# Optimization experiments

Hardware: AMD Instinct MI355X
Metric: run time of the kernel (lower is better)

## Reference

```python
import jax, jax.numpy as jnp
import numpy as np

B, A, NBH, F, G, H = 8, 512, 64, 128, 50, 8
DH = F // H
CUTOFF = 5.0


def setup_inputs() -> dict:
    key = jax.random.key(0)
    ks = jax.random.split(key, 13)
    x = jax.random.normal(ks[0], (B, A, F), jnp.float32)
    e = jax.random.normal(ks[1], (B, A, F), jnp.float32)
    t = jax.random.normal(ks[2], (B, F), jnp.float32)
    # distances in [0, 1.2*cutoff] so some pairs fall outside the cutoff
    r_ij = jax.random.uniform(ks[3], (B, A, NBH), jnp.float32) * (1.2 * CUTOFF)
    f_ij = jax.random.normal(ks[4], (B, A, NBH, G), jnp.float32)
    neighbors = jax.random.randint(ks[5], (B, A, NBH), 0, A, jnp.int32)
    neighbor_mask = jax.random.randint(ks[6], (B, A, NBH), 0, 2, jnp.int32).astype(bool)
    sF = 1.0 / np.sqrt(F).astype(np.float32)
    W_filt = jax.random.normal(ks[7], (G, F), jnp.float32) * (1.0 / np.sqrt(G).astype(np.float32))
    b_filt = jnp.zeros((F,), jnp.float32)
    Wq = jax.random.normal(ks[8], (F, F), jnp.float32) * sF
    Wk = jax.random.normal(ks[9], (F, F), jnp.float32) * sF
    Wv = jax.random.normal(ks[10], (F, F), jnp.float32) * sF
    Wo = jax.random.normal(ks[11], (F, F), jnp.float32) * sF
    bo = jnp.zeros((F,), jnp.float32)
    return dict(e=e, x=x, t=t, r_ij=r_ij, f_ij=f_ij,
                W_filt=W_filt, b_filt=b_filt, Wq=Wq, Wk=Wk, Wv=Wv, Wo=Wo, bo=bo,
                neighbors=neighbors, neighbor_mask=neighbor_mask)


def reference(e, x, t, r_ij, f_ij, W_filt, b_filt, Wq, Wk, Wv, Wo, bo,
              neighbors, neighbor_mask):
    # ---- filter network + cosine cutoff: W (B, A, NBH, F) ----
    W = f_ij @ W_filt + b_filt
    C = 0.5 * (jnp.cos(jnp.pi * r_ij / CUTOFF) + 1.0)
    C = C * (r_ij < CUTOFF).astype(x.dtype)           # (B, A, NBH)
    W = W * C[..., None]

    # ---- neighbor gather: nbh (B, A, NBH, F) ----
    bidx = jnp.arange(B)[:, None, None]
    nbh = x[bidx, neighbors]                           # irregular gather
    nbh = nbh * W                                      # filter-modulated messages

    # ---- EgoAttention: central atom queries its neighbors ----
    q = (x @ Wq).reshape(B, A, H, DH)                  # bahd
    k = (nbh @ Wk).reshape(B, A, NBH, H, DH)           # banhd
    v = (nbh @ Wv).reshape(B, A, NBH, H, DH)
    scale = np.float32(1.0 / np.sqrt(DH))
    scores = jnp.einsum('bahd,banhd->bahn', q, k) * scale
    scores = jnp.where(neighbor_mask[:, :, None, :], scores, jnp.float32(-1e9))
    attn = jax.nn.softmax(scores, axis=-1)             # over neighbors
    msg = jnp.einsum('bahn,banhd->bahd', attn, v).reshape(B, A, F)
    v_out = msg @ Wo + bo

    # ---- residual (apply_transition_function=False branch) ----
    return x + v_out
```

## Files before the change

kernel.cpp:

```cpp
#include <hip/hip_runtime.h>
#include <math.h>

#define BB 8
#define AA 512
#define NBH 64
#define FF 128
#define GG 50
#define NH 8
#define DH 16
#define CUTOFF 5.0f

typedef __attribute__((ext_vector_type(8))) short bf16x8;
typedef __attribute__((ext_vector_type(4))) float f32x4;

#define MST 136
#define FST 72

#define W4_ELEMS (8*4*64*8)
#define W2_ELEMS (8*2*64*8)

__device__ __forceinline__ short f2bf(float f) {
    union { float f; unsigned u; } v; v.f = f;
    unsigned r = v.u + 0x7fffu + ((v.u >> 16) & 1u);
    return (short)(r >> 16);
}

__global__ void prep_kernel(const float* __restrict__ Wk,
                            const float* __restrict__ Wv,
                            const float* __restrict__ Wq,
                            const float* __restrict__ Wo,
                            const float* __restrict__ Wf,
                            short* __restrict__ ws)
{
    int gid = blockIdx.x * blockDim.x + threadIdx.x;
    if (gid < 4 * W4_ELEMS) {
        int m = gid >> 14;
        const float* src = (m == 0) ? Wk : (m == 1) ? Wv : (m == 2) ? Wq : Wo;
        int idx = gid & (W4_ELEMS - 1);
        int jj  = idx & 7;
        int l   = (idx >> 3) & 63;
        int cs  = idx >> 9;
        int s   = cs & 3, c = cs >> 2;
        int k   = s * 32 + (l >> 4) * 8 + jj;
        int n   = c * 16 + (l & 15);
        ws[gid] = f2bf(src[k * FF + n]);
    } else if (gid < 4 * W4_ELEMS + W2_ELEMS) {
        int idx = gid - 4 * W4_ELEMS;
        int jj  = idx & 7;
        int l   = (idx >> 3) & 63;
        int cs  = idx >> 9;
        int s   = cs & 1, c = cs >> 1;
        int g   = s * 32 + (l >> 4) * 8 + jj;
        int n   = c * 16 + (l & 15);
        ws[gid] = (g < GG) ? f2bf(Wf[g * FF + n]) : (short)0;
    }
}

__global__ __launch_bounds__(256, 4)
void tdt_main(const float* __restrict__ x,
              const float* __restrict__ r_ij,
              const float* __restrict__ f_ij,
              const float* __restrict__ b_filt,
              const float* __restrict__ bo,
              const int*   __restrict__ neighbors,
              const int*   __restrict__ nmask,
              const short* __restrict__ WkB,
              const short* __restrict__ WvB,
              const short* __restrict__ WqB,
              const short* __restrict__ WoB,
              const short* __restrict__ WfB,
              float* __restrict__ out)
{
    const int ba   = blockIdx.x;
    const int b    = ba >> 9;
    const int tid  = threadIdx.x;
    const int lane = tid & 63;
    const int w    = tid >> 6;
    const int l15  = lane & 15;
    const int quad = lane >> 4;

    __shared__ short M_s[NBH * MST];
    __shared__ short f_s[NBH * FST];
    __shared__ short x_bf[FF];
    __shared__ short msg_bf[FF];
    __shared__ float x_s[FF];
    __shared__ float C_s[NBH];
    __shared__ int   nbr_s[NBH];
    __shared__ int   mask_s[NBH];

    const float* xb  = x + (size_t)b * AA * FF;
    const size_t bao = (size_t)ba;

    if (tid < FF) {
        float xv = x[bao * FF + tid];
        x_s[tid]  = xv;
        x_bf[tid] = f2bf(xv);
    }
    if (tid < NBH) {
        float r = r_ij[bao * NBH + tid];
        float c = 0.5f * (cosf((float)M_PI * r * (1.0f / CUTOFF)) + 1.0f);
        C_s[tid]    = (r < CUTOFF) ? c : 0.0f;
        nbr_s[tid]  = neighbors[bao * NBH + tid];
        mask_s[tid] = nmask[bao * NBH + tid];
    }
    {
        const float* frow = f_ij + bao * (size_t)(NBH * GG);
        for (int idx = tid; idx < NBH * GG; idx += 256) {
            int n = idx / GG;
            int g = idx - n * GG;
            f_s[n * FST + g] = f2bf(frow[idx]);
        }
        for (int idx = tid; idx < NBH * (64 - GG); idx += 256) {
            int n = idx / (64 - GG);
            int g = GG + (idx - n * (64 - GG));
            f_s[n * FST + g] = 0;
        }
    }
    __syncthreads();

    float qv[2];
    {
        bf16x8 xa[4];
#pragma unroll
        for (int s = 0; s < 4; ++s)
            xa[s] = *(const bf16x8*)&x_bf[s * 32 + quad * 8];
#pragma unroll
        for (int ct = 0; ct < 2; ++ct) {
            int cg = 2 * w + ct;
            f32x4 z = {0.f, 0.f, 0.f, 0.f};
#pragma unroll
            for (int s = 0; s < 4; ++s) {
                bf16x8 bq = *(const bf16x8*)&WqB[((cg * 4 + s) * 64 + lane) * 8];
                z = __builtin_amdgcn_mfma_f32_16x16x32_bf16(xa[s], bq, z, 0, 0, 0);
            }
            qv[ct] = z[0];
        }
    }

    {
        f32x4 wacc[2][4];
        {
            bf16x8 fa[4][2];
#pragma unroll
            for (int mt = 0; mt < 4; ++mt)
#pragma unroll
                for (int s = 0; s < 2; ++s)
                    fa[mt][s] = *(const bf16x8*)&f_s[(16 * mt + l15) * FST + s * 32 + quad * 8];
#pragma unroll
            for (int ct = 0; ct < 2; ++ct) {
                int cg = 2 * w + ct;
                bf16x8 b0 = *(const bf16x8*)&WfB[((cg * 2 + 0) * 64 + lane) * 8];
                bf16x8 b1 = *(const bf16x8*)&WfB[((cg * 2 + 1) * 64 + lane) * 8];
#pragma unroll
                for (int mt = 0; mt < 4; ++mt) {
                    f32x4 z = {0.f, 0.f, 0.f, 0.f};
                    z = __builtin_amdgcn_mfma_f32_16x16x32_bf16(fa[mt][0], b0, z, 0, 0, 0);
                    z = __builtin_amdgcn_mfma_f32_16x16x32_bf16(fa[mt][1], b1, z, 0, 0, 0);
                    wacc[ct][mt] = z;
                }
            }
        }
        int   c0  = (2 * w + 0) * 16 + l15;
        int   c1  = (2 * w + 1) * 16 + l15;
        float bf0 = b_filt[c0];
        float bf1 = b_filt[c1];
#pragma unroll
        for (int mt = 0; mt < 4; ++mt) {
#pragma unroll
            for (int r = 0; r < 4; ++r) {
                int n = 16 * mt + quad * 4 + r;
                float cn = C_s[n];
                const float* xrow = xb + (size_t)nbr_s[n] * FF;
                M_s[n * MST + c0] = f2bf((wacc[0][mt][r] + bf0) * cn * xrow[c0]);
                M_s[n * MST + c1] = f2bf((wacc[1][mt][r] + bf1) * cn * xrow[c1]);
            }
        }
    }
    __syncthreads();

#pragma unroll
    for (int ct = 0; ct < 2; ++ct) {
        int cg = 2 * w + ct;
        bf16x8 bk[4], bv[4];
#pragma unroll
        for (int s = 0; s < 4; ++s) {
            bk[s] = *(const bf16x8*)&WkB[((cg * 4 + s) * 64 + lane) * 8];
            bv[s] = *(const bf16x8*)&WvB[((cg * 4 + s) * 64 + lane) * 8];
        }
        f32x4 kacc[4], vacc[4];
#pragma unroll
        for (int mt = 0; mt < 4; ++mt) {
            f32x4 zk = {0.f, 0.f, 0.f, 0.f}, zv = {0.f, 0.f, 0.f, 0.f};
#pragma unroll
            for (int s = 0; s < 4; ++s) {
                bf16x8 ma = *(const bf16x8*)&M_s[(16 * mt + l15) * MST + s * 32 + quad * 8];
                zk = __builtin_amdgcn_mfma_f32_16x16x32_bf16(ma, bk[s], zk, 0, 0, 0);
                zv = __builtin_amdgcn_mfma_f32_16x16x32_bf16(ma, bv[s], zv, 0, 0, 0);
            }
            kacc[mt] = zk; vacc[mt] = zv;
        }
        float sc[4][4];
#pragma unroll
        for (int mt = 0; mt < 4; ++mt) {
#pragma unroll
            for (int r = 0; r < 4; ++r) {
                float s = kacc[mt][r] * qv[ct];
                s += __shfl_xor(s, 1, 64);
                s += __shfl_xor(s, 2, 64);
                s += __shfl_xor(s, 4, 64);
                s += __shfl_xor(s, 8, 64);
                int n = 16 * mt + quad * 4 + r;
                s *= 0.25f;
                if (!mask_s[n]) s = -1e9f;
                sc[mt][r] = s;
            }
        }
        float m = sc[0][0];
#pragma unroll
        for (int mt = 0; mt < 4; ++mt)
#pragma unroll
            for (int r = 0; r < 4; ++r) m = fmaxf(m, sc[mt][r]);
        m = fmaxf(m, __shfl_xor(m, 16, 64));
        m = fmaxf(m, __shfl_xor(m, 32, 64));
        float sum = 0.0f;
#pragma unroll
        for (int mt = 0; mt < 4; ++mt)
#pragma unroll
            for (int r = 0; r < 4; ++r) {
                sc[mt][r] = __expf(sc[mt][r] - m);
                sum += sc[mt][r];
            }
        sum += __shfl_xor(sum, 16, 64);
        sum += __shfl_xor(sum, 32, 64);
        float inv = 1.0f / sum;
        float acc = 0.0f;
#pragma unroll
        for (int mt = 0; mt < 4; ++mt)
#pragma unroll
            for (int r = 0; r < 4; ++r)
                acc = fmaf(sc[mt][r], vacc[mt][r], acc);
        acc += __shfl_xor(acc, 16, 64);
        acc += __shfl_xor(acc, 32, 64);
        if (quad == 0) msg_bf[cg * 16 + l15] = f2bf(acc * inv);
    }
    __syncthreads();

    {
        bf16x8 mga[4];
#pragma unroll
        for (int s = 0; s < 4; ++s)
            mga[s] = *(const bf16x8*)&msg_bf[s * 32 + quad * 8];
#pragma unroll
        for (int ct = 0; ct < 2; ++ct) {
            int cg = 2 * w + ct;
            f32x4 z = {0.f, 0.f, 0.f, 0.f};
#pragma unroll
            for (int s = 0; s < 4; ++s) {
                bf16x8 bw = *(const bf16x8*)&WoB[((cg * 4 + s) * 64 + lane) * 8];
                z = __builtin_amdgcn_mfma_f32_16x16x32_bf16(mga[s], bw, z, 0, 0, 0);
            }
            if (quad == 0) {
                int col = cg * 16 + l15;
                out[bao * FF + col] = z[0] + x_s[col] + bo[col];
            }
        }
    }
}

extern "C" void kernel_launch(void* const* d_in, const int* in_sizes, int n_in,
                              void* d_out, int out_size, void* d_ws, size_t ws_size,
                              hipStream_t stream) {
    const float* x      = (const float*)d_in[1];
    const float* r_ij   = (const float*)d_in[3];
    const float* f_ij   = (const float*)d_in[4];
    const float* W_filt = (const float*)d_in[5];
    const float* b_filt = (const float*)d_in[6];
    const float* Wq     = (const float*)d_in[7];
    const float* Wk     = (const float*)d_in[8];
    const float* Wv     = (const float*)d_in[9];
    const float* Wo     = (const float*)d_in[10];
    const float* bo     = (const float*)d_in[11];
    const int*   nbr    = (const int*)d_in[12];
    const int*   msk    = (const int*)d_in[13];
    float* out = (float*)d_out;

    short* ws = (short*)d_ws;
    short* WkB = ws;
    short* WvB = ws + W4_ELEMS;
    short* WqB = ws + 2 * W4_ELEMS;
    short* WoB = ws + 3 * W4_ELEMS;
    short* WfB = ws + 4 * W4_ELEMS;

    int prep_total = 4 * W4_ELEMS + W2_ELEMS;
    hipLaunchKernelGGL(prep_kernel, dim3((prep_total + 255) / 256), dim3(256), 0, stream,
                       Wk, Wv, Wq, Wo, W_filt, ws);
    hipLaunchKernelGGL(tdt_main, dim3(BB * AA), dim3(256), 0, stream,
                       x, r_ij, f_ij, b_filt, bo, nbr, msk,
                       WkB, WvB, WqB, WoB, WfB, out);
}
```

Baseline: 166.9 us.

## Switch filter and K/V projections to 32x32x16 MFMA with swizzled LDS

```diff
diff --git a/kernel.cpp b/kernel.cpp
--- a/kernel.cpp
+++ b/kernel.cpp
@@ -6,23 +6,34 @@
 #define NBH 64
 #define FF 128
 #define GG 50
-#define NH 8
-#define DH 16
 #define CUTOFF 5.0f
 
-typedef __attribute__((ext_vector_type(8))) short bf16x8;
-typedef __attribute__((ext_vector_type(4))) float f32x4;
+typedef __attribute__((ext_vector_type(8)))  short bf16x8;
+typedef __attribute__((ext_vector_type(4)))  float f32x4;
+typedef __attribute__((ext_vector_type(16))) float f32x16;
 
 #define MST 136
 #define FST 72
 
-#define W4_ELEMS (8*4*64*8)
-#define W2_ELEMS (8*2*64*8)
+#define WKV_ELEMS (4*8*64*8)
+#define WQO_ELEMS (8*4*64*8)
+#define WF_ELEMS  (4*4*64*8)
 
 __device__ __forceinline__ short f2bf(float f) {
     union { float f; unsigned u; } v; v.f = f;
     unsigned r = v.u + 0x7fffu + ((v.u >> 16) & 1u);
     return (short)(r >> 16);
+}
+
+__device__ __forceinline__ int swz(int n) { return ((n >> 3) & 3) << 3; }
+
+__device__ __forceinline__ float row16_sum(float x) {
+    int t;
+    t = __builtin_amdgcn_update_dpp(0, __float_as_int(x), 0x128, 0xf, 0xf, true); x += __int_as_float(t);
+    t = __builtin_amdgcn_update_dpp(0, __float_as_int(x), 0x124, 0xf, 0xf, true); x += __int_as_float(t);
+    t = __builtin_amdgcn_update_dpp(0, __float_as_int(x), 0x122, 0xf, 0xf, true); x += __int_as_float(t);
+    t = __builtin_amdgcn_update_dpp(0, __float_as_int(x), 0x121, 0xf, 0xf, true); x += __int_as_float(t);
+    return x;
 }
 
 __global__ void prep_kernel(const float* __restrict__ Wk,
@@ -33,26 +44,30 @@
                             short* __restrict__ ws)
 {
     int gid = blockIdx.x * blockDim.x + threadIdx.x;
-    if (gid < 4 * W4_ELEMS) {
-        int m = gid >> 14;
-        const float* src = (m == 0) ? Wk : (m == 1) ? Wv : (m == 2) ? Wq : Wo;
-        int idx = gid & (W4_ELEMS - 1);
-        int jj  = idx & 7;
-        int l   = (idx >> 3) & 63;
-        int cs  = idx >> 9;
-        int s   = cs & 3, c = cs >> 2;
-        int k   = s * 32 + (l >> 4) * 8 + jj;
-        int n   = c * 16 + (l & 15);
+    if (gid < 2 * WKV_ELEMS) {
+        const float* src = (gid < WKV_ELEMS) ? Wk : Wv;
+        int idx = gid & (WKV_ELEMS - 1);
+        int j = idx & 7, l = (idx >> 3) & 63, rest = idx >> 9;
+        int s = rest & 7, w = rest >> 3;
+        int k = 16 * s + ((l >> 5) << 3) + j;
+        int n = 32 * w + (l & 31);
         ws[gid] = f2bf(src[k * FF + n]);
-    } else if (gid < 4 * W4_ELEMS + W2_ELEMS) {
-        int idx = gid - 4 * W4_ELEMS;
-        int jj  = idx & 7;
-        int l   = (idx >> 3) & 63;
-        int cs  = idx >> 9;
-        int s   = cs & 1, c = cs >> 1;
-        int g   = s * 32 + (l >> 4) * 8 + jj;
-        int n   = c * 16 + (l & 15);
-        ws[gid] = (g < GG) ? f2bf(Wf[g * FF + n]) : (short)0;
+    } else if (gid < 2 * WKV_ELEMS + 2 * WQO_ELEMS) {
+        int idx2 = gid - 2 * WKV_ELEMS;
+        const float* src = (idx2 < WQO_ELEMS) ? Wq : Wo;
+        int idx = idx2 & (WQO_ELEMS - 1);
+        int j = idx & 7, l = (idx >> 3) & 63, rest = idx >> 9;
+        int s = rest & 3, c = rest >> 2;
+        int k = 32 * s + (l >> 4) * 8 + j;
+        int n = 16 * c + (l & 15);
+        ws[gid] = f2bf(src[k * FF + n]);
+    } else {
+        int idx = gid - 2 * WKV_ELEMS - 2 * WQO_ELEMS;
+        int j = idx & 7, l = (idx >> 3) & 63, rest = idx >> 9;
+        int s = rest & 3, w = rest >> 2;
+        int k = 16 * s + ((l >> 5) << 3) + j;
+        int n = 32 * w + (l & 31);
+        ws[gid] = (k < GG) ? f2bf(Wf[k * FF + n]) : (short)0;
     }
 }
 
@@ -78,6 +93,8 @@
     const int w    = tid >> 6;
     const int l15  = lane & 15;
     const int quad = lane >> 4;
+    const int l31  = lane & 31;
+    const int w5_4 = (lane >> 5) * 4;
 
     __shared__ short M_s[NBH * MST];
     __shared__ short f_s[NBH * FST];
@@ -86,10 +103,11 @@
     __shared__ float x_s[FF];
     __shared__ float C_s[NBH];
     __shared__ int   nbr_s[NBH];
-    __shared__ int   mask_s[NBH];
 
     const float* xb  = x + (size_t)b * AA * FF;
     const size_t bao = (size_t)ba;
+
+    unsigned long long mask64 = __ballot(nmask[bao * NBH + lane] != 0);
 
     if (tid < FF) {
         float xv = x[bao * FF + tid];
@@ -98,22 +116,25 @@
     }
     if (tid < NBH) {
         float r = r_ij[bao * NBH + tid];
-        float c = 0.5f * (cosf((float)M_PI * r * (1.0f / CUTOFF)) + 1.0f);
-        C_s[tid]    = (r < CUTOFF) ? c : 0.0f;
-        nbr_s[tid]  = neighbors[bao * NBH + tid];
-        mask_s[tid] = nmask[bao * NBH + tid];
+        float c = 0.5f * (__cosf((float)M_PI * r * (1.0f / CUTOFF)) + 1.0f);
+        C_s[tid]   = (r < CUTOFF) ? c : 0.0f;
+        nbr_s[tid] = neighbors[bao * NBH + tid];
     }
     {
         const float* frow = f_ij + bao * (size_t)(NBH * GG);
-        for (int idx = tid; idx < NBH * GG; idx += 256) {
-            int n = idx / GG;
-            int g = idx - n * GG;
-            f_s[n * FST + g] = f2bf(frow[idx]);
+        int n = tid / 50;
+        int g = tid - n * 50;
+        for (int it = 0; it < 13; ++it) {
+            int idx = tid + it * 256;
+            if (idx < NBH * GG)
+                f_s[n * FST + (g ^ swz(n))] = f2bf(frow[idx]);
+            g += 6; n += 5;
+            if (g >= 50) { g -= 50; n += 1; }
         }
         for (int idx = tid; idx < NBH * (64 - GG); idx += 256) {
-            int n = idx / (64 - GG);
-            int g = GG + (idx - n * (64 - GG));
-            f_s[n * FST + g] = 0;
+            int nn = idx / 14;
+            int gg = GG + (idx - nn * 14);
+            f_s[nn * FST + (gg ^ swz(nn))] = 0;
         }
     }
     __syncthreads();
@@ -138,110 +159,95 @@
     }
 
     {
-        f32x4 wacc[2][4];
-        {
-            bf16x8 fa[4][2];
-#pragma unroll
-            for (int mt = 0; mt < 4; ++mt)
-#pragma unroll
-                for (int s = 0; s < 2; ++s)
-                    fa[mt][s] = *(const bf16x8*)&f_s[(16 * mt + l15) * FST + s * 32 + quad * 8];
-#pragma unroll
-            for (int ct = 0; ct < 2; ++ct) {
-                int cg = 2 * w + ct;
-                bf16x8 b0 = *(const bf16x8*)&WfB[((cg * 2 + 0) * 64 + lane) * 8];
-                bf16x8 b1 = *(const bf16x8*)&WfB[((cg * 2 + 1) * 64 + lane) * 8];
-#pragma unroll
-                for (int mt = 0; mt < 4; ++mt) {
-                    f32x4 z = {0.f, 0.f, 0.f, 0.f};
-                    z = __builtin_amdgcn_mfma_f32_16x16x32_bf16(fa[mt][0], b0, z, 0, 0, 0);
-                    z = __builtin_amdgcn_mfma_f32_16x16x32_bf16(fa[mt][1], b1, z, 0, 0, 0);
-                    wacc[ct][mt] = z;
-                }
-            }
-        }
-        int   c0  = (2 * w + 0) * 16 + l15;
-        int   c1  = (2 * w + 1) * 16 + l15;
-        float bf0 = b_filt[c0];
-        float bf1 = b_filt[c1];
-#pragma unroll
-        for (int mt = 0; mt < 4; ++mt) {
-#pragma unroll
-            for (int r = 0; r < 4; ++r) {
-                int n = 16 * mt + quad * 4 + r;
+        f32x16 wacc[2];
+#pragma unroll
+        for (int mt = 0; mt < 2; ++mt)
+#pragma unroll
+            for (int r = 0; r < 16; ++r) wacc[mt][r] = 0.0f;
+#pragma unroll
+        for (int s = 0; s < 4; ++s) {
+            bf16x8 bf = *(const bf16x8*)&WfB[((w * 4 + s) * 64 + lane) * 8];
+            int kb = 16 * s + ((lane >> 5) << 3);
+#pragma unroll
+            for (int mt = 0; mt < 2; ++mt) {
+                int m = 32 * mt + l31;
+                bf16x8 fa = *(const bf16x8*)&f_s[m * FST + (kb ^ swz(m))];
+                wacc[mt] = __builtin_amdgcn_mfma_f32_32x32x16_bf16(fa, bf, wacc[mt], 0, 0, 0);
+            }
+        }
+        int   c    = 32 * w + l31;
+        float bflt = b_filt[c];
+#pragma unroll
+        for (int mt = 0; mt < 2; ++mt) {
+#pragma unroll
+            for (int r = 0; r < 16; ++r) {
+                int n = 32 * mt + (r & 3) + 8 * (r >> 2) + w5_4;
                 float cn = C_s[n];
-                const float* xrow = xb + (size_t)nbr_s[n] * FF;
-                M_s[n * MST + c0] = f2bf((wacc[0][mt][r] + bf0) * cn * xrow[c0]);
-                M_s[n * MST + c1] = f2bf((wacc[1][mt][r] + bf1) * cn * xrow[c1]);
+                float xv = xb[(size_t)nbr_s[n] * FF + c];
+                M_s[n * MST + (c ^ swz(n))] = f2bf((wacc[mt][r] + bflt) * cn * xv);
             }
         }
     }
     __syncthreads();
 
-#pragma unroll
-    for (int ct = 0; ct < 2; ++ct) {
-        int cg = 2 * w + ct;
-        bf16x8 bk[4], bv[4];
-#pragma unroll
-        for (int s = 0; s < 4; ++s) {
-            bk[s] = *(const bf16x8*)&WkB[((cg * 4 + s) * 64 + lane) * 8];
-            bv[s] = *(const bf16x8*)&WvB[((cg * 4 + s) * 64 + lane) * 8];
-        }
-        f32x4 kacc[4], vacc[4];
-#pragma unroll
-        for (int mt = 0; mt < 4; ++mt) {
-            f32x4 zk = {0.f, 0.f, 0.f, 0.f}, zv = {0.f, 0.f, 0.f, 0.f};
-#pragma unroll
-            for (int s = 0; s < 4; ++s) {
-                bf16x8 ma = *(const bf16x8*)&M_s[(16 * mt + l15) * MST + s * 32 + quad * 8];
-                zk = __builtin_amdgcn_mfma_f32_16x16x32_bf16(ma, bk[s], zk, 0, 0, 0);
-                zv = __builtin_amdgcn_mfma_f32_16x16x32_bf16(ma, bv[s], zv, 0, 0, 0);
-            }
-            kacc[mt] = zk; vacc[mt] = zv;
-        }
-        float sc[4][4];
-#pragma unroll
-        for (int mt = 0; mt < 4; ++mt) {
-#pragma unroll
-            for (int r = 0; r < 4; ++r) {
-                float s = kacc[mt][r] * qv[ct];
-                s += __shfl_xor(s, 1, 64);
-                s += __shfl_xor(s, 2, 64);
-                s += __shfl_xor(s, 4, 64);
-                s += __shfl_xor(s, 8, 64);
-                int n = 16 * mt + quad * 4 + r;
+    f32x16 kacc[2], vacc[2];
+#pragma unroll
+    for (int mt = 0; mt < 2; ++mt)
+#pragma unroll
+        for (int r = 0; r < 16; ++r) { kacc[mt][r] = 0.0f; vacc[mt][r] = 0.0f; }
+#pragma unroll
+    for (int s = 0; s < 8; ++s) {
+        bf16x8 bk = *(const bf16x8*)&WkB[((w * 8 + s) * 64 + lane) * 8];
+        bf16x8 bv = *(const bf16x8*)&WvB[((w * 8 + s) * 64 + lane) * 8];
+        int kb = 16 * s + ((lane >> 5) << 3);
+#pragma unroll
+        for (int mt = 0; mt < 2; ++mt) {
+            int m = 32 * mt + l31;
+            bf16x8 ma = *(const bf16x8*)&M_s[m * MST + (kb ^ swz(m))];
+            kacc[mt] = __builtin_amdgcn_mfma_f32_32x32x16_bf16(ma, bk, kacc[mt], 0, 0, 0);
+            vacc[mt] = __builtin_amdgcn_mfma_f32_32x32x16_bf16(ma, bv, vacc[mt], 0, 0, 0);
+        }
+    }
+
+    {
+        float qvm = qv[(lane >> 4) & 1];
+        float sc[2][16];
+#pragma unroll
+        for (int mt = 0; mt < 2; ++mt) {
+#pragma unroll
+            for (int r = 0; r < 16; ++r) {
+                float s = kacc[mt][r] * qvm;
+                s = row16_sum(s);
+                int n = 32 * mt + (r & 3) + 8 * (r >> 2) + w5_4;
                 s *= 0.25f;
-                if (!mask_s[n]) s = -1e9f;
-                sc[mt][r] = s;
-            }
-        }
-        float m = sc[0][0];
-#pragma unroll
-        for (int mt = 0; mt < 4; ++mt)
-#pragma unroll
-            for (int r = 0; r < 4; ++r) m = fmaxf(m, sc[mt][r]);
-        m = fmaxf(m, __shfl_xor(m, 16, 64));
-        m = fmaxf(m, __shfl_xor(m, 32, 64));
+                sc[mt][r] = ((mask64 >> n) & 1ull) ? s : -1e9f;
+            }
+        }
+        float mx = -1e30f;
+#pragma unroll
+        for (int mt = 0; mt < 2; ++mt)
+#pragma unroll
+            for (int r = 0; r < 16; ++r) mx = fmaxf(mx, sc[mt][r]);
+        mx = fmaxf(mx, __shfl_xor(mx, 32, 64));
         float sum = 0.0f;
 #pragma unroll
-        for (int mt = 0; mt < 4; ++mt)
-#pragma unroll
-            for (int r = 0; r < 4; ++r) {
-                sc[mt][r] = __expf(sc[mt][r] - m);
-                sum += sc[mt][r];
-            }
-        sum += __shfl_xor(sum, 16, 64);
+        for (int mt = 0; mt < 2; ++mt)
+#pragma unroll
+            for (int r = 0; r < 16; ++r) {
+                float e = __expf(sc[mt][r] - mx);
+                sc[mt][r] = e;
+                sum += e;
+            }
         sum += __shfl_xor(sum, 32, 64);
         float inv = 1.0f / sum;
         float acc = 0.0f;
 #pragma unroll
-        for (int mt = 0; mt < 4; ++mt)
-#pragma unroll
-            for (int r = 0; r < 4; ++r)
+        for (int mt = 0; mt < 2; ++mt)
+#pragma unroll
+            for (int r = 0; r < 16; ++r)
                 acc = fmaf(sc[mt][r], vacc[mt][r], acc);
-        acc += __shfl_xor(acc, 16, 64);
         acc += __shfl_xor(acc, 32, 64);
-        if (quad == 0) msg_bf[cg * 16 + l15] = f2bf(acc * inv);
+        if (lane < 32) msg_bf[32 * w + l31] = f2bf(acc * inv);
     }
     __syncthreads();
 
@@ -284,15 +290,15 @@
     const int*   msk    = (const int*)d_in[13];
     float* out = (float*)d_out;
 
-    short* ws = (short*)d_ws;
+    short* ws  = (short*)d_ws;
     short* WkB = ws;
-    short* WvB = ws + W4_ELEMS;
-    short* WqB = ws + 2 * W4_ELEMS;
-    short* WoB = ws + 3 * W4_ELEMS;
-    short* WfB = ws + 4 * W4_ELEMS;
-
-    int prep_total = 4 * W4_ELEMS + W2_ELEMS;
-    hipLaunchKernelGGL(prep_kernel, dim3((prep_total + 255) / 256), dim3(256), 0, stream,
+    short* WvB = ws + WKV_ELEMS;
+    short* WqB = ws + 2 * WKV_ELEMS;
+    short* WoB = ws + 2 * WKV_ELEMS + WQO_ELEMS;
+    short* WfB = ws + 2 * WKV_ELEMS + 2 * WQO_ELEMS;
+
+    int prep_total = 2 * WKV_ELEMS + 2 * WQO_ELEMS + WF_ELEMS;
+    hipLaunchKernelGGL(prep_kernel, dim3(prep_total / 256), dim3(256), 0, stream,
                        Wk, Wv, Wq, Wo, W_filt, ws);
     hipLaunchKernelGGL(tdt_main, dim3(BB * AA), dim3(256), 0, stream,
                        x, r_ij, f_ij, b_filt, bo, nbr, msk,
```

After: 176.9 us. +6.0%, slower.
